# Performance work log

Hardware: AMD Instinct MI355X
Metric: run time of the kernel (lower is better)

## Reference

```python
import jax, jax.numpy as jnp
import numpy as np

N_LEVELS = 16
N_FEATS = 2
LOG2_T = 19
BASE_RES = 16.0
FINEST_RES = 512.0
BOX_MIN = jnp.array([-1.0, -1.0, -1.0], dtype=jnp.float32)
BOX_MAX = jnp.array([1.0, 1.0, 1.0], dtype=jnp.float32)
# corner offsets, i (x) slowest, k (z) fastest -> index = 4*i + 2*j + k, matching BOX_OFFSETS
OFFSETS = jnp.array([[i, j, k] for i in (0, 1) for j in (0, 1) for k in (0, 1)], dtype=jnp.int32)  # [8,3]
PRIMES = jnp.array([73856093, 19349663, 83492791], dtype=jnp.int32)
HASH_MASK = (1 << LOG2_T) - 1


def setup_inputs() -> dict:
    key = jax.random.key(0)
    k1, k2 = jax.random.split(key)
    B = 1_000_000
    # points inside the bounding box
    x = jax.random.uniform(k1, (B, 3), dtype=jnp.float32, minval=-1.0, maxval=1.0)
    # nn.init.uniform_(w, a=-1e-4, b=1e-4)
    embeddings = jax.random.uniform(k2, (N_LEVELS, 1 << LOG2_T, N_FEATS), dtype=jnp.float32,
                                    minval=-1e-4, maxval=1e-4)
    return {"x": x, "embeddings": embeddings}


def _hash_encode(x, embeddings):
    # x: [B,3], embeddings: [L,T,F]
    b = jnp.exp((jnp.log(FINEST_RES) - jnp.log(BASE_RES)) / (N_LEVELS - 1))
    resolutions = jnp.floor(BASE_RES * b ** jnp.arange(N_LEVELS, dtype=jnp.float32))  # [L]
    xc = jnp.clip(x, BOX_MIN, BOX_MAX)

    def level_fn(table, res):
        grid_size = (BOX_MAX - BOX_MIN) / res  # [3]
        bl = jnp.floor((xc - BOX_MIN) / grid_size).astype(jnp.int32)  # [B,3]
        vmin = bl.astype(xc.dtype) * grid_size + BOX_MIN               # [B,3]
        w = (xc - vmin) / grid_size                                    # [B,3] in [0,1]
        idx = bl[:, None, :] + OFFSETS[None, :, :]                     # [B,8,3]
        prod = idx * PRIMES                                            # int32 wraparound, as in torch
        h = (prod[..., 0] ^ prod[..., 1] ^ prod[..., 2]) & HASH_MASK   # [B,8] in [0,2^19)
        emb = table[h]                                                 # [B,8,F] gather
        # trilinear weights: prod_d (o_d*w_d + (1-o_d)*(1-w_d))
        cw = jnp.prod(jnp.where(OFFSETS[None].astype(bool), w[:, None, :], 1.0 - w[:, None, :]), axis=-1)  # [B,8]
        return jnp.sum(cw[..., None] * emb, axis=1)                    # [B,F]

    outs = jax.vmap(level_fn)(embeddings, resolutions)                 # [L,B,F]
    B = x.shape[0]
    return jnp.transpose(outs, (1, 0, 2)).reshape(B, N_LEVELS * N_FEATS)


def reference(x, embeddings):
    return _hash_encode(x, embeddings)
```

## Files before the change

kernel.cpp:

```cpp
#include <hip/hip_runtime.h>
#include <stdint.h>

#define TMASK ((1u << 19) - 1u)
#define EMB_SCALE     8192.0f
#define EMB_INV_SCALE (1.0f / 8192.0f)

typedef float    vf2 __attribute__((ext_vector_type(2)));
typedef float    vf4 __attribute__((ext_vector_type(4)));
typedef _Float16 vh2 __attribute__((ext_vector_type(2)));
typedef _Float16 vh4 __attribute__((ext_vector_type(4)));

static __device__ const float GS_F[16] = {
    2.0f/16.0f, 2.0f/20.0f, 2.0f/25.0f, 2.0f/32.0f,
    2.0f/40.0f, 2.0f/50.0f, 2.0f/64.0f, 2.0f/80.0f,
    2.0f/101.0f, 2.0f/128.0f, 2.0f/161.0f, 2.0f/203.0f,
    2.0f/256.0f, 2.0f/322.0f, 2.0f/406.0f, 2.0f/512.0f};
static __device__ const float INVGS_F[16] = {
    8.0f, 10.0f, 12.5f, 16.0f,
    20.0f, 25.0f, 32.0f, 40.0f,
    50.5f, 64.0f, 80.5f, 101.5f,
    128.0f, 161.0f, 203.0f, 256.0f};

#define N_L0 4913
#define N_L1 9261
#define N_L2 17576
#define N_L3 35937
#define DENSE_OFF1 (N_L0)
#define DENSE_OFF2 (N_L0 + N_L1)
#define DENSE_OFF3 (N_L0 + N_L1 + N_L2)
#define DENSE_TOT  (N_L0 + N_L1 + N_L2 + N_L3)

static __device__ const int REMAP_S[4]   = {17, 21, 26, 33};
static __device__ const int REMAP_N[4]   = {N_L0, N_L1, N_L2, N_L3};
static __device__ const int REMAP_OFF[4] = {0, DENSE_OFF1, DENSE_OFF2, DENSE_OFF3};

struct Corner8 { vf2 e[8]; float w[8]; };

__device__ __forceinline__ vf2 load_entry(const vf2* __restrict__ tb, uint32_t h) {
    return tb[h];
}
__device__ __forceinline__ vf2 load_entry(const vh2* __restrict__ tb, uint32_t h) {
    const vh2 v = tb[h];
    vf2 r; r.x = (float)v.x; r.y = (float)v.y;
    return r;
}

template <typename T>
__device__ __forceinline__ void gather_level(
    const T* __restrict__ tb, float cx, float cy, float cz,
    float gs, float ivg, Corner8& g)
{
    const float ux = (cx + 1.0f) * ivg;
    const float uy = (cy + 1.0f) * ivg;
    const float uz = (cz + 1.0f) * ivg;
    const float fx = floorf(ux), fy = floorf(uy), fz = floorf(uz);
    const int ix = (int)fx, iy = (int)fy, iz = (int)fz;
    const float wx = (cx - (fx * gs - 1.0f)) * ivg;
    const float wy = (cy - (fy * gs - 1.0f)) * ivg;
    const float wz = (cz - (fz * gs - 1.0f)) * ivg;

    const uint32_t px0 = (uint32_t)ix * 73856093u, px1 = px0 + 73856093u;
    const uint32_t py0 = (uint32_t)iy * 19349663u, py1 = py0 + 19349663u;
    const uint32_t pz0 = (uint32_t)iz * 83492791u, pz1 = pz0 + 83492791u;

    g.e[0] = load_entry(tb, (px0 ^ py0 ^ pz0) & TMASK);
    g.e[1] = load_entry(tb, (px0 ^ py0 ^ pz1) & TMASK);
    g.e[2] = load_entry(tb, (px0 ^ py1 ^ pz0) & TMASK);
    g.e[3] = load_entry(tb, (px0 ^ py1 ^ pz1) & TMASK);
    g.e[4] = load_entry(tb, (px1 ^ py0 ^ pz0) & TMASK);
    g.e[5] = load_entry(tb, (px1 ^ py0 ^ pz1) & TMASK);
    g.e[6] = load_entry(tb, (px1 ^ py1 ^ pz0) & TMASK);
    g.e[7] = load_entry(tb, (px1 ^ py1 ^ pz1) & TMASK);

    const float wxm = 1.0f - wx, wym = 1.0f - wy, wzm = 1.0f - wz;
    const float c00 = wxm * wym, c01 = wxm * wy;
    const float c10 = wx  * wym, c11 = wx  * wy;
    g.w[0] = c00 * wzm; g.w[1] = c00 * wz;
    g.w[2] = c01 * wzm; g.w[3] = c01 * wz;
    g.w[4] = c10 * wzm; g.w[5] = c10 * wz;
    g.w[6] = c11 * wzm; g.w[7] = c11 * wz;
}

__device__ __forceinline__ vf2 blend(const Corner8& g) {
    vf2 r;
    r.x = g.w[0]*g.e[0].x + g.w[1]*g.e[1].x + g.w[2]*g.e[2].x + g.w[3]*g.e[3].x
        + g.w[4]*g.e[4].x + g.w[5]*g.e[5].x + g.w[6]*g.e[6].x + g.w[7]*g.e[7].x;
    r.y = g.w[0]*g.e[0].y + g.w[1]*g.e[1].y + g.w[2]*g.e[2].y + g.w[3]*g.e[3].y
        + g.w[4]*g.e[4].y + g.w[5]*g.e[5].y + g.w[6]*g.e[6].y + g.w[7]*g.e[7].y;
    return r;
}

__global__ __launch_bounds__(256) void convert_kernel(
    const vf4* __restrict__ emb, vh4* __restrict__ tb, int n4)
{
    const int i = blockIdx.x * blockDim.x + threadIdx.x;
    if (i >= n4) return;
    const vf4 v = __builtin_nontemporal_load(emb + i);
    vh4 o;
    o.x = (_Float16)(v.x * EMB_SCALE);
    o.y = (_Float16)(v.y * EMB_SCALE);
    o.z = (_Float16)(v.z * EMB_SCALE);
    o.w = (_Float16)(v.w * EMB_SCALE);
    tb[i] = o;
}

__global__ __launch_bounds__(256) void remap_kernel(
    const vf2* __restrict__ emb, vh2* __restrict__ dense)
{
    const int l = blockIdx.y;
    const int S = REMAP_S[l];
    const int n = REMAP_N[l];
    const int d = blockIdx.x * 256 + threadIdx.x;
    if (d >= n) return;
    const int jz = d % S;
    const int r  = d / S;
    const int jy = r % S;
    const int jx = r / S;
    const uint32_t h = ((uint32_t)jx * 73856093u
                      ^ (uint32_t)jy * 19349663u
                      ^ (uint32_t)jz * 83492791u) & TMASK;
    const vf2 e = emb[((size_t)l << 19) + h];
    vh2 o; o.x = (_Float16)(e.x * EMB_SCALE); o.y = (_Float16)(e.y * EMB_SCALE);
    dense[REMAP_OFF[l] + d] = o;
}

__device__ __forceinline__ vf2 unpack_u32(uint32_t r) {
    const vh2 v = __builtin_bit_cast(vh2, r);
    vf2 o; o.x = (float)v.x; o.y = (float)v.y;
    return o;
}

template <int RES>
__device__ __forceinline__ vf2 coarse_point(
    const uint32_t* __restrict__ tb, float cx, float cy, float cz)
{
    constexpr int S = RES + 1, S2 = S * S;
    constexpr float gs  = 2.0f / (float)RES;
    constexpr float ivg = (float)RES * 0.5f;

    const float ux = (cx + 1.0f) * ivg;
    const float uy = (cy + 1.0f) * ivg;
    const float uz = (cz + 1.0f) * ivg;
    const float fx = floorf(ux), fy = floorf(uy), fz = floorf(uz);
    const int ix = (int)fx, iy = (int)fy, iz = (int)fz;
    const float wx = (cx - (fx * gs - 1.0f)) * ivg;
    const float wy = (cy - (fy * gs - 1.0f)) * ivg;
    const float wz = (cz - (fz * gs - 1.0f)) * ivg;
    const int d0 = (ix * S + iy) * S + iz;

    const vf2 e0 = unpack_u32(tb[d0]);
    const vf2 e1 = unpack_u32(tb[d0 + 1]);
    const vf2 e2 = unpack_u32(tb[d0 + S]);
    const vf2 e3 = unpack_u32(tb[d0 + S + 1]);
    const vf2 e4 = unpack_u32(tb[d0 + S2]);
    const vf2 e5 = unpack_u32(tb[d0 + S2 + 1]);
    const vf2 e6 = unpack_u32(tb[d0 + S2 + S]);
    const vf2 e7 = unpack_u32(tb[d0 + S2 + S + 1]);

    const float wxm = 1.0f - wx, wym = 1.0f - wy, wzm = 1.0f - wz;
    const float c00 = wxm * wym, c01 = wxm * wy;
    const float c10 = wx  * wym, c11 = wx  * wy;
    const float w0 = c00 * wzm, w1 = c00 * wz, w2 = c01 * wzm, w3 = c01 * wz;
    const float w4 = c10 * wzm, w5 = c10 * wz, w6 = c11 * wzm, w7 = c11 * wz;

    vf2 r;
    r.x = w0*e0.x + w1*e1.x + w2*e2.x + w3*e3.x
        + w4*e4.x + w5*e5.x + w6*e6.x + w7*e7.x;
    r.y = w0*e0.y + w1*e1.y + w2*e2.y + w3*e3.y
        + w4*e4.y + w5*e5.y + w6*e6.y + w7*e7.y;
    r.x *= EMB_INV_SCALE; r.y *= EMB_INV_SCALE;
    return r;
}

template <int LA, int LB, int CMODE, int NT>
__global__ __launch_bounds__(NT) void pair_kernel(
    const float* __restrict__ x,
    const vh2* __restrict__ tbl,
    const uint32_t* __restrict__ dense,
    vf2* __restrict__ ws,
    int B, int half)
{
    extern __shared__ uint32_t lds[];
    if constexpr (CMODE == 1) {
        for (int i = threadIdx.x; i < N_L0 + N_L1; i += NT) lds[i] = dense[i];
        __syncthreads();
    } else if constexpr (CMODE == 2) {
        for (int i = threadIdx.x; i < N_L2; i += NT) lds[i] = dense[DENSE_OFF2 + i];
        __syncthreads();
    } else if constexpr (CMODE == 3) {
        for (int i = threadIdx.x; i < N_L3; i += NT) lds[i] = dense[DENSE_OFF3 + i];
        __syncthreads();
    }

    const int p0 = blockIdx.x * NT + threadIdx.x;
    if (p0 >= half) return;
    const int p1 = p0 + half;
    const bool has1 = p1 < B;
    const int p1c = has1 ? p1 : p0;

    const float ax = __builtin_nontemporal_load(x + 3*p0 + 0);
    const float ay = __builtin_nontemporal_load(x + 3*p0 + 1);
    const float az = __builtin_nontemporal_load(x + 3*p0 + 2);
    const float bx = __builtin_nontemporal_load(x + 3*p1c + 0);
    const float by = __builtin_nontemporal_load(x + 3*p1c + 1);
    const float bz = __builtin_nontemporal_load(x + 3*p1c + 2);

    const float cax = fminf(fmaxf(ax, -1.0f), 1.0f);
    const float cay = fminf(fmaxf(ay, -1.0f), 1.0f);
    const float caz = fminf(fmaxf(az, -1.0f), 1.0f);
    const float cbx = fminf(fmaxf(bx, -1.0f), 1.0f);
    const float cby = fminf(fmaxf(by, -1.0f), 1.0f);
    const float cbz = fminf(fmaxf(bz, -1.0f), 1.0f);

    const vh2* __restrict__ tbA = tbl + ((size_t)LA << 19);
    const vh2* __restrict__ tbB = tbl + ((size_t)LB << 19);
    Corner8 gaA, gbA, gaB, gbB;
    gather_level(tbA, cax, cay, caz, GS_F[LA], INVGS_F[LA], gaA);
    gather_level(tbA, cbx, cby, cbz, GS_F[LA], INVGS_F[LA], gbA);
    gather_level(tbB, cax, cay, caz, GS_F[LB], INVGS_F[LB], gaB);
    gather_level(tbB, cbx, cby, cbz, GS_F[LB], INVGS_F[LB], gbB);

    if constexpr (CMODE == 1) {
        const vf2 a0 = coarse_point<16>(lds, cax, cay, caz);
        const vf2 b0 = coarse_point<16>(lds, cbx, cby, cbz);
        const vf2 a1 = coarse_point<20>(lds + N_L0, cax, cay, caz);
        const vf2 b1 = coarse_point<20>(lds + N_L0, cbx, cby, cbz);
        __builtin_nontemporal_store(a0, &ws[p0]);
        if (has1) __builtin_nontemporal_store(b0, &ws[p1]);
        __builtin_nontemporal_store(a1, &ws[(long)B + p0]);
        if (has1) __builtin_nontemporal_store(b1, &ws[(long)B + p1]);
    } else if constexpr (CMODE == 2) {
        const vf2 a2 = coarse_point<25>(lds, cax, cay, caz);
        const vf2 b2 = coarse_point<25>(lds, cbx, cby, cbz);
        __builtin_nontemporal_store(a2, &ws[(long)2 * B + p0]);
        if (has1) __builtin_nontemporal_store(b2, &ws[(long)2 * B + p1]);
    } else if constexpr (CMODE == 3) {
        const vf2 a3 = coarse_point<32>(lds, cax, cay, caz);
        const vf2 b3 = coarse_point<32>(lds, cbx, cby, cbz);
        __builtin_nontemporal_store(a3, &ws[(long)3 * B + p0]);
        if (has1) __builtin_nontemporal_store(b3, &ws[(long)3 * B + p1]);
    }

    vf2 raA = blend(gaA), rbA = blend(gbA);
    vf2 raB = blend(gaB), rbB = blend(gbB);
    raA.x *= EMB_INV_SCALE; raA.y *= EMB_INV_SCALE;
    rbA.x *= EMB_INV_SCALE; rbA.y *= EMB_INV_SCALE;
    raB.x *= EMB_INV_SCALE; raB.y *= EMB_INV_SCALE;
    rbB.x *= EMB_INV_SCALE; rbB.y *= EMB_INV_SCALE;

    __builtin_nontemporal_store(raA, &ws[(long)LA * B + p0]);
    if (has1) __builtin_nontemporal_store(rbA, &ws[(long)LA * B + p1]);
    __builtin_nontemporal_store(raB, &ws[(long)LB * B + p0]);
    if (has1) __builtin_nontemporal_store(rbB, &ws[(long)LB * B + p1]);
}

__global__ __launch_bounds__(256) void transpose_kernel(
    const vf2* __restrict__ ws, vf4* __restrict__ out, int B)
{
    __shared__ vf2 tile[16][257];
    const int t = threadIdx.x;
    const int base = blockIdx.x * 256;

#pragma unroll
    for (int l = 0; l < 16; ++l) {
        const int b = base + t;
        if (b < B) tile[l][t] = __builtin_nontemporal_load(&ws[(long)l * B + b]);
    }
    __syncthreads();

#pragma unroll
    for (int k = 0; k < 8; ++k) {
        const int flat = k * 256 + t;
        const int p = flat >> 3;
        const int j = flat & 7;
        if (base + p < B) {
            const vf2 a = tile[2*j][p];
            const vf2 c = tile[2*j+1][p];
            vf4 v; v.x = a.x; v.y = a.y; v.z = c.x; v.w = c.y;
            __builtin_nontemporal_store(v, &out[(long)base * 8 + flat]);
        }
    }
}

__global__ __launch_bounds__(256) void monolith_kernel(
    const float* __restrict__ x,
    const vf2* __restrict__ tbl,
    vf4* __restrict__ out,
    int B, int half)
{
    const int t = threadIdx.x;
    const int base = blockIdx.x * 256;
    const int p0r = base + t;
    const int p0 = p0r < half ? p0r : half - 1;
    const int p1r = p0 + half;
    const int p1 = p1r < B ? p1r : B - 1;

    const float cax = fminf(fmaxf(__builtin_nontemporal_load(x + 3*p0 + 0), -1.0f), 1.0f);
    const float cay = fminf(fmaxf(__builtin_nontemporal_load(x + 3*p0 + 1), -1.0f), 1.0f);
    const float caz = fminf(fmaxf(__builtin_nontemporal_load(x + 3*p0 + 2), -1.0f), 1.0f);
    const float cbx = fminf(fmaxf(__builtin_nontemporal_load(x + 3*p1 + 0), -1.0f), 1.0f);
    const float cby = fminf(fmaxf(__builtin_nontemporal_load(x + 3*p1 + 1), -1.0f), 1.0f);
    const float cbz = fminf(fmaxf(__builtin_nontemporal_load(x + 3*p1 + 2), -1.0f), 1.0f);

    vf2 oa[16], ob[16];
#pragma unroll
    for (int l = 0; l < 16; ++l) {
        const vf2* __restrict__ tb = tbl + ((size_t)l << 19);
        Corner8 ga, gb;
        gather_level(tb, cax, cay, caz, GS_F[l], INVGS_F[l], ga);
        gather_level(tb, cbx, cby, cbz, GS_F[l], INVGS_F[l], gb);
        oa[l] = blend(ga); ob[l] = blend(gb);
    }

    __shared__ vf2 tile[16][257];
#pragma unroll
    for (int l = 0; l < 16; ++l) tile[l][t] = oa[l];
    __syncthreads();
#pragma unroll
    for (int k = 0; k < 8; ++k) {
        const int flat = k * 256 + t;
        const int p = flat >> 3;
        const int j = flat & 7;
        if (base + p < half) {
            const vf2 a = tile[2*j][p];
            const vf2 c = tile[2*j+1][p];
            vf4 v; v.x = a.x; v.y = a.y; v.z = c.x; v.w = c.y;
            __builtin_nontemporal_store(v, &out[(long)(base + p) * 8 + j]);
        }
    }
    __syncthreads();
#pragma unroll
    for (int l = 0; l < 16; ++l) tile[l][t] = ob[l];
    __syncthreads();
#pragma unroll
    for (int k = 0; k < 8; ++k) {
        const int flat = k * 256 + t;
        const int p = flat >> 3;
        const int j = flat & 7;
        const long pt = (long)base + half + p;
        if (pt < B) {
            const vf2 a = tile[2*j][p];
            const vf2 c = tile[2*j+1][p];
            vf4 v; v.x = a.x; v.y = a.y; v.z = c.x; v.w = c.y;
            __builtin_nontemporal_store(v, &out[pt * 8 + j]);
        }
    }
}

extern "C" void kernel_launch(void* const* d_in, const int* in_sizes, int n_in,
                              void* d_out, int out_size, void* d_ws, size_t ws_size,
                              hipStream_t stream) {
    const float* x   = (const float*)d_in[0];
    const float* emb = (const float*)d_in[1];
    const int B = in_sizes[0] / 3;

    const int half = (B + 1) / 2;
    const size_t tbl_bytes = (size_t)16 * 524288 * sizeof(vh2);
    const size_t ws_bytes  = (size_t)B * 16 * sizeof(vf2);
    const size_t dense_bytes = (size_t)DENSE_TOT * sizeof(vh2);

    if (ws_size >= tbl_bytes + ws_bytes && (size_t)out_size >= dense_bytes) {
        vh2* tb = (vh2*)d_ws;
        vf2* ws = (vf2*)((char*)d_ws + tbl_bytes);
        vh2* dense = (vh2*)d_out;
        const uint32_t* dn = (const uint32_t*)dense;

        static int attr_done = 0;
        if (!attr_done) {
            (void)hipFuncSetAttribute(
                reinterpret_cast<const void*>(&pair_kernel<4, 5, 1, 1024>),
                hipFuncAttributeMaxDynamicSharedMemorySize, (N_L0 + N_L1) * 4);
            (void)hipFuncSetAttribute(
                reinterpret_cast<const void*>(&pair_kernel<6, 7, 2, 1024>),
                hipFuncAttributeMaxDynamicSharedMemorySize, N_L2 * 4);
            (void)hipFuncSetAttribute(
                reinterpret_cast<const void*>(&pair_kernel<8, 9, 3, 1024>),
                hipFuncAttributeMaxDynamicSharedMemorySize, N_L3 * 4);
            attr_done = 1;
        }

        const int n4 = 16 * 524288 * 2 / 4;
        convert_kernel<<<(n4 + 255) / 256, 256, 0, stream>>>(
            (const vf4*)emb, (vh4*)tb, n4);
        remap_kernel<<<dim3((N_L3 + 255) / 256, 4), 256, 0, stream>>>(
            (const vf2*)emb, dense);

        const int g1024 = (half + 1023) / 1024;
        const int g256  = (half + 255) / 256;
        pair_kernel<4, 5, 1, 1024><<<g1024, 1024, (N_L0 + N_L1) * 4, stream>>>(
            x, tb, dn, ws, B, half);
        pair_kernel<6, 7, 2, 1024><<<g1024, 1024, N_L2 * 4, stream>>>(
            x, tb, dn, ws, B, half);
        pair_kernel<8, 9, 3, 1024><<<g1024, 1024, N_L3 * 4, stream>>>(
            x, tb, dn, ws, B, half);
        pair_kernel<10, 11, 0, 256><<<g256, 256, 0, stream>>>(
            x, tb, dn, ws, B, half);
        pair_kernel<12, 13, 0, 256><<<g256, 256, 0, stream>>>(
            x, tb, dn, ws, B, half);
        pair_kernel<14, 15, 0, 256><<<g256, 256, 0, stream>>>(
            x, tb, dn, ws, B, half);

        transpose_kernel<<<(B + 255) / 256, 256, 0, stream>>>(ws, (vf4*)d_out, B);
    } else {
        const int grid = (half + 255) / 256;
        monolith_kernel<<<grid, 256, 0, stream>>>(
            x, (const vf2*)emb, (vf4*)d_out, B, half);
    }
}
```

Measured before the change: 660.7 us.

## Sort points by Morton bin and scatter results directly to output

Adds a counting sort of points into 32768 Morton-ordered spatial bins (histogram, scan, scatter) so that neighbouring threads in the per-level pair kernels touch nearby hash/dense table entries, improving cache locality of the gathers. The pair kernels now read packed sorted points and write their results straight to the final output rows, removing the per-level workspace and the transpose kernel. The dense coarse tables move from the output buffer into workspace. It costs extra passes over x, atomics, and scattered 16-byte output writes.

```diff
diff --git a/kernel.cpp b/kernel.cpp
--- a/kernel.cpp
+++ b/kernel.cpp
@@ -30,6 +30,8 @@
 #define DENSE_OFF3 (N_L0 + N_L1 + N_L2)
 #define DENSE_TOT  (N_L0 + N_L1 + N_L2 + N_L3)
 
+#define NBINS 32768
+
 static __device__ const int REMAP_S[4]   = {17, 21, 26, 33};
 static __device__ const int REMAP_N[4]   = {N_L0, N_L1, N_L2, N_L3};
 static __device__ const int REMAP_OFF[4] = {0, DENSE_OFF1, DENSE_OFF2, DENSE_OFF3};
@@ -88,6 +90,69 @@
     r.y = g.w[0]*g.e[0].y + g.w[1]*g.e[1].y + g.w[2]*g.e[2].y + g.w[3]*g.e[3].y
         + g.w[4]*g.e[4].y + g.w[5]*g.e[5].y + g.w[6]*g.e[6].y + g.w[7]*g.e[7].y;
     return r;
+}
+
+__device__ __forceinline__ uint32_t spread5(uint32_t v) {
+    v &= 31u;
+    v = (v | (v << 8)) & 0x0000100Fu;
+    v = (v | (v << 4)) & 0x000010C3u;
+    v = (v | (v << 2)) & 0x00001249u;
+    return v;
+}
+__device__ __forceinline__ uint32_t morton_key(float cx, float cy, float cz) {
+    const int bx = min((int)((cx + 1.0f) * 16.0f), 31);
+    const int by = min((int)((cy + 1.0f) * 16.0f), 31);
+    const int bz = min((int)((cz + 1.0f) * 16.0f), 31);
+    return spread5((uint32_t)bx) | (spread5((uint32_t)by) << 1)
+         | (spread5((uint32_t)bz) << 2);
+}
+
+__global__ __launch_bounds__(1024) void zero_kernel(uint32_t* h, int n) {
+    const int i = blockIdx.x * 1024 + threadIdx.x;
+    if (i < n) h[i] = 0u;
+}
+
+__global__ __launch_bounds__(256) void hist_kernel(
+    const float* __restrict__ x, uint32_t* __restrict__ hist, int B)
+{
+    const int p = blockIdx.x * 256 + threadIdx.x;
+    if (p >= B) return;
+    const float cx = fminf(fmaxf(x[3*p+0], -1.0f), 1.0f);
+    const float cy = fminf(fmaxf(x[3*p+1], -1.0f), 1.0f);
+    const float cz = fminf(fmaxf(x[3*p+2], -1.0f), 1.0f);
+    atomicAdd(&hist[morton_key(cx, cy, cz)], 1u);
+}
+
+__global__ __launch_bounds__(1024) void scan_kernel(
+    const uint32_t* __restrict__ hist, uint32_t* __restrict__ cursor)
+{
+    __shared__ uint32_t part[1024];
+    const int t = threadIdx.x;
+    uint32_t loc[32];
+    uint32_t s = 0;
+#pragma unroll
+    for (int i = 0; i < 32; ++i) { loc[i] = s; s += hist[t * 32 + i]; }
+    part[t] = s;
+    __syncthreads();
+    uint32_t acc = 0;
+    for (int i = 0; i < t; ++i) acc += part[i];
+#pragma unroll
+    for (int i = 0; i < 32; ++i) cursor[t * 32 + i] = acc + loc[i];
+}
+
+__global__ __launch_bounds__(256) void scatter_kernel(
+    const float* __restrict__ x, uint32_t* __restrict__ cursor,
+    vf4* __restrict__ sorted, int B)
+{
+    const int p = blockIdx.x * 256 + threadIdx.x;
+    if (p >= B) return;
+    const float cx = fminf(fmaxf(x[3*p+0], -1.0f), 1.0f);
+    const float cy = fminf(fmaxf(x[3*p+1], -1.0f), 1.0f);
+    const float cz = fminf(fmaxf(x[3*p+2], -1.0f), 1.0f);
+    const uint32_t pos = atomicAdd(&cursor[morton_key(cx, cy, cz)], 1u);
+    vf4 v; v.x = cx; v.y = cy; v.z = cz;
+    v.w = __uint_as_float((uint32_t)p);
+    __builtin_nontemporal_store(v, &sorted[pos]);
 }
 
 __global__ __launch_bounds__(256) void convert_kernel(
@@ -174,10 +239,10 @@
 
 template <int LA, int LB, int CMODE, int NT>
 __global__ __launch_bounds__(NT) void pair_kernel(
-    const float* __restrict__ x,
+    const vf4* __restrict__ sorted,
     const vh2* __restrict__ tbl,
     const uint32_t* __restrict__ dense,
-    vf2* __restrict__ ws,
+    float* __restrict__ out,
     int B, int half)
 {
     extern __shared__ uint32_t lds[];
@@ -198,19 +263,12 @@
     const bool has1 = p1 < B;
     const int p1c = has1 ? p1 : p0;
 
-    const float ax = __builtin_nontemporal_load(x + 3*p0 + 0);
-    const float ay = __builtin_nontemporal_load(x + 3*p0 + 1);
-    const float az = __builtin_nontemporal_load(x + 3*p0 + 2);
-    const float bx = __builtin_nontemporal_load(x + 3*p1c + 0);
-    const float by = __builtin_nontemporal_load(x + 3*p1c + 1);
-    const float bz = __builtin_nontemporal_load(x + 3*p1c + 2);
-
-    const float cax = fminf(fmaxf(ax, -1.0f), 1.0f);
-    const float cay = fminf(fmaxf(ay, -1.0f), 1.0f);
-    const float caz = fminf(fmaxf(az, -1.0f), 1.0f);
-    const float cbx = fminf(fmaxf(bx, -1.0f), 1.0f);
-    const float cby = fminf(fmaxf(by, -1.0f), 1.0f);
-    const float cbz = fminf(fmaxf(bz, -1.0f), 1.0f);
+    const vf4 A = __builtin_nontemporal_load(&sorted[p0]);
+    const vf4 Bv = __builtin_nontemporal_load(&sorted[p1c]);
+    const float cax = A.x,  cay = A.y,  caz = A.z;
+    const float cbx = Bv.x, cby = Bv.y, cbz = Bv.z;
+    const uint32_t ia = __float_as_uint(A.w);
+    const uint32_t ib = __float_as_uint(Bv.w);
 
     const vh2* __restrict__ tbA = tbl + ((size_t)LA << 19);
     const vh2* __restrict__ tbB = tbl + ((size_t)LB << 19);
@@ -220,65 +278,49 @@
     gather_level(tbB, cax, cay, caz, GS_F[LB], INVGS_F[LB], gaB);
     gather_level(tbB, cbx, cby, cbz, GS_F[LB], INVGS_F[LB], gbB);
 
+    vf2 c0a, c0b, c1a, c1b;
     if constexpr (CMODE == 1) {
-        const vf2 a0 = coarse_point<16>(lds, cax, cay, caz);
-        const vf2 b0 = coarse_point<16>(lds, cbx, cby, cbz);
-        const vf2 a1 = coarse_point<20>(lds + N_L0, cax, cay, caz);
-        const vf2 b1 = coarse_point<20>(lds + N_L0, cbx, cby, cbz);
-        __builtin_nontemporal_store(a0, &ws[p0]);
-        if (has1) __builtin_nontemporal_store(b0, &ws[p1]);
-        __builtin_nontemporal_store(a1, &ws[(long)B + p0]);
-        if (has1) __builtin_nontemporal_store(b1, &ws[(long)B + p1]);
+        c0a = coarse_point<16>(lds, cax, cay, caz);
+        c0b = coarse_point<16>(lds, cbx, cby, cbz);
+        c1a = coarse_point<20>(lds + N_L0, cax, cay, caz);
+        c1b = coarse_point<20>(lds + N_L0, cbx, cby, cbz);
     } else if constexpr (CMODE == 2) {
-        const vf2 a2 = coarse_point<25>(lds, cax, cay, caz);
-        const vf2 b2 = coarse_point<25>(lds, cbx, cby, cbz);
-        __builtin_nontemporal_store(a2, &ws[(long)2 * B + p0]);
-        if (has1) __builtin_nontemporal_store(b2, &ws[(long)2 * B + p1]);
+        c0a = coarse_point<25>(lds, cax, cay, caz);
+        c0b = coarse_point<25>(lds, cbx, cby, cbz);
     } else if constexpr (CMODE == 3) {
-        const vf2 a3 = coarse_point<32>(lds, cax, cay, caz);
-        const vf2 b3 = coarse_point<32>(lds, cbx, cby, cbz);
-        __builtin_nontemporal_store(a3, &ws[(long)3 * B + p0]);
-        if (has1) __builtin_nontemporal_store(b3, &ws[(long)3 * B + p1]);
-    }
-
-    vf2 raA = blend(gaA), rbA = blend(gbA);
-    vf2 raB = blend(gaB), rbB = blend(gbB);
-    raA.x *= EMB_INV_SCALE; raA.y *= EMB_INV_SCALE;
-    rbA.x *= EMB_INV_SCALE; rbA.y *= EMB_INV_SCALE;
-    raB.x *= EMB_INV_SCALE; raB.y *= EMB_INV_SCALE;
-    rbB.x *= EMB_INV_SCALE; rbB.y *= EMB_INV_SCALE;
-
-    __builtin_nontemporal_store(raA, &ws[(long)LA * B + p0]);
-    if (has1) __builtin_nontemporal_store(rbA, &ws[(long)LA * B + p1]);
-    __builtin_nontemporal_store(raB, &ws[(long)LB * B + p0]);
-    if (has1) __builtin_nontemporal_store(rbB, &ws[(long)LB * B + p1]);
-}
-
-__global__ __launch_bounds__(256) void transpose_kernel(
-    const vf2* __restrict__ ws, vf4* __restrict__ out, int B)
-{
-    __shared__ vf2 tile[16][257];
-    const int t = threadIdx.x;
-    const int base = blockIdx.x * 256;
-
-#pragma unroll
-    for (int l = 0; l < 16; ++l) {
-        const int b = base + t;
-        if (b < B) tile[l][t] = __builtin_nontemporal_load(&ws[(long)l * B + b]);
-    }
-    __syncthreads();
-
-#pragma unroll
-    for (int k = 0; k < 8; ++k) {
-        const int flat = k * 256 + t;
-        const int p = flat >> 3;
-        const int j = flat & 7;
-        if (base + p < B) {
-            const vf2 a = tile[2*j][p];
-            const vf2 c = tile[2*j+1][p];
-            vf4 v; v.x = a.x; v.y = a.y; v.z = c.x; v.w = c.y;
-            __builtin_nontemporal_store(v, &out[(long)base * 8 + flat]);
+        c0a = coarse_point<32>(lds, cax, cay, caz);
+        c0b = coarse_point<32>(lds, cbx, cby, cbz);
+    }
+
+    vf2 rA = blend(gaA), rB = blend(gaB);
+    vf2 sA = blend(gbA), sB = blend(gbB);
+    constexpr int slot = LA / 2;
+    {
+        vf4 v; v.x = rA.x * EMB_INV_SCALE; v.y = rA.y * EMB_INV_SCALE;
+        v.z = rB.x * EMB_INV_SCALE; v.w = rB.y * EMB_INV_SCALE;
+        __builtin_nontemporal_store(v, (vf4*)(out + (size_t)ia * 32 + slot * 4));
+    }
+    if (has1) {
+        vf4 v; v.x = sA.x * EMB_INV_SCALE; v.y = sA.y * EMB_INV_SCALE;
+        v.z = sB.x * EMB_INV_SCALE; v.w = sB.y * EMB_INV_SCALE;
+        __builtin_nontemporal_store(v, (vf4*)(out + (size_t)ib * 32 + slot * 4));
+    }
+
+    if constexpr (CMODE == 1) {
+        vf4 v; v.x = c0a.x; v.y = c0a.y; v.z = c1a.x; v.w = c1a.y;
+        __builtin_nontemporal_store(v, (vf4*)(out + (size_t)ia * 32));
+        if (has1) {
+            vf4 w; w.x = c0b.x; w.y = c0b.y; w.z = c1b.x; w.w = c1b.y;
+            __builtin_nontemporal_store(w, (vf4*)(out + (size_t)ib * 32));
         }
+    } else if constexpr (CMODE == 2) {
+        __builtin_nontemporal_store(c0a, (vf2*)(out + (size_t)ia * 32 + 4));
+        if (has1)
+            __builtin_nontemporal_store(c0b, (vf2*)(out + (size_t)ib * 32 + 4));
+    } else if constexpr (CMODE == 3) {
+        __builtin_nontemporal_store(c0a, (vf2*)(out + (size_t)ia * 32 + 6));
+        if (has1)
+            __builtin_nontemporal_store(c0b, (vf2*)(out + (size_t)ib * 32 + 6));
     }
 }
 
@@ -355,14 +397,22 @@
     const int B = in_sizes[0] / 3;
 
     const int half = (B + 1) / 2;
-    const size_t tbl_bytes = (size_t)16 * 524288 * sizeof(vh2);
-    const size_t ws_bytes  = (size_t)B * 16 * sizeof(vf2);
-    const size_t dense_bytes = (size_t)DENSE_TOT * sizeof(vh2);
-
-    if (ws_size >= tbl_bytes + ws_bytes && (size_t)out_size >= dense_bytes) {
-        vh2* tb = (vh2*)d_ws;
-        vf2* ws = (vf2*)((char*)d_ws + tbl_bytes);
-        vh2* dense = (vh2*)d_out;
+
+    const size_t tbl_bytes    = (size_t)16 * 524288 * sizeof(vh2);
+    const size_t sorted_off   = tbl_bytes;
+    const size_t sorted_bytes = (size_t)B * sizeof(vf4);
+    const size_t hist_off     = sorted_off + sorted_bytes;
+    const size_t hist_bytes   = (size_t)NBINS * 4;
+    const size_t cursor_off   = hist_off + hist_bytes;
+    const size_t dense_off    = cursor_off + hist_bytes;
+    const size_t need         = dense_off + (size_t)DENSE_TOT * sizeof(vh2);
+
+    if (ws_size >= need) {
+        vh2* tb          = (vh2*)d_ws;
+        vf4* sorted      = (vf4*)((char*)d_ws + sorted_off);
+        uint32_t* hist   = (uint32_t*)((char*)d_ws + hist_off);
+        uint32_t* cursor = (uint32_t*)((char*)d_ws + cursor_off);
+        vh2* dense       = (vh2*)((char*)d_ws + dense_off);
         const uint32_t* dn = (const uint32_t*)dense;
 
         static int attr_done = 0;
@@ -379,28 +429,33 @@
             attr_done = 1;
         }
 
+        const int gB = (B + 255) / 256;
+
         const int n4 = 16 * 524288 * 2 / 4;
         convert_kernel<<<(n4 + 255) / 256, 256, 0, stream>>>(
             (const vf4*)emb, (vh4*)tb, n4);
         remap_kernel<<<dim3((N_L3 + 255) / 256, 4), 256, 0, stream>>>(
             (const vf2*)emb, dense);
 
+        zero_kernel<<<(NBINS + 1023) / 1024, 1024, 0, stream>>>(hist, NBINS);
+        hist_kernel<<<gB, 256, 0, stream>>>(x, hist, B);
+        scan_kernel<<<1, 1024, 0, stream>>>(hist, cursor);
+        scatter_kernel<<<gB, 256, 0, stream>>>(x, cursor, sorted, B);
+
         const int g1024 = (half + 1023) / 1024;
         const int g256  = (half + 255) / 256;
         pair_kernel<4, 5, 1, 1024><<<g1024, 1024, (N_L0 + N_L1) * 4, stream>>>(
-            x, tb, dn, ws, B, half);
+            sorted, tb, dn, (float*)d_out, B, half);
         pair_kernel<6, 7, 2, 1024><<<g1024, 1024, N_L2 * 4, stream>>>(
-            x, tb, dn, ws, B, half);
+            sorted, tb, dn, (float*)d_out, B, half);
         pair_kernel<8, 9, 3, 1024><<<g1024, 1024, N_L3 * 4, stream>>>(
-            x, tb, dn, ws, B, half);
+            sorted, tb, dn, (float*)d_out, B, half);
         pair_kernel<10, 11, 0, 256><<<g256, 256, 0, stream>>>(
-            x, tb, dn, ws, B, half);
+            sorted, tb, dn, (float*)d_out, B, half);
         pair_kernel<12, 13, 0, 256><<<g256, 256, 0, stream>>>(
-            x, tb, dn, ws, B, half);
+            sorted, tb, dn, (float*)d_out, B, half);
         pair_kernel<14, 15, 0, 256><<<g256, 256, 0, stream>>>(
-            x, tb, dn, ws, B, half);
-
-        transpose_kernel<<<(B + 255) / 256, 256, 0, stream>>>(ws, (vf4*)d_out, B);
+            sorted, tb, dn, (float*)d_out, B, half);
     } else {
         const int grid = (half + 255) / 256;
         monolith_kernel<<<grid, 256, 0, stream>>>(
```

After: 893.9 us. 35.3% more time.
